# Performance work log

Hardware: AMD Instinct MI355X
Metric: run time of the kernel (lower is better)

Reference implementation:

```python
import jax, jax.numpy as jnp
import numpy as np

META_DIM, CIN, COUT, K = 32, 64, 64, 3
B, N, S = 32, 256, 64


def setup_inputs() -> dict:
    key = jax.random.key(0)
    k1, k2, k3, k4, k5, k6 = jax.random.split(key, 6)
    scale = 1.0 / np.sqrt(META_DIM)
    return {
        "meta_knowledge": jax.random.normal(k1, (B, N, META_DIM), dtype=jnp.float32),
        "x": jax.random.normal(k2, (B, N, S, CIN), dtype=jnp.float32),
        "w_lin_w": jax.random.normal(k3, (CIN * COUT * K, META_DIM), dtype=jnp.float32) * scale,
        "w_lin_b": jax.random.normal(k4, (CIN * COUT * K,), dtype=jnp.float32) * scale,
        "b_lin_w": jax.random.normal(k5, (COUT, META_DIM), dtype=jnp.float32) * scale,
        "b_lin_b": jax.random.normal(k6, (COUT,), dtype=jnp.float32) * scale,
    }


def reference(meta_knowledge, x, w_lin_w, w_lin_b, b_lin_w, b_lin_b):
    # meta_knowledge: [B, N, M]; x: [B, N, S, Cin]
    b, n, s, cin = x.shape
    cout = b_lin_w.shape[0]
    k = w_lin_w.shape[0] // (cin * cout)
    s_out = s - k + 1

    # Hypernetwork: per-(batch,node) conv weights and biases
    # w: [B, N, Cout, Cin, K]
    w = (jnp.einsum("bnm,pm->bnp", meta_knowledge, w_lin_w) + w_lin_b)
    w = w.reshape(b, n, cout, cin, k)
    # bias: [B, N, Cout]
    bias = jnp.einsum("bnm,om->bno", meta_knowledge, b_lin_w) + b_lin_b

    # Sliding windows over seq axis (valid conv): [B, N, S_out, K, Cin]
    x_win = jnp.stack([x[:, :, j : j + s_out, :] for j in range(k)], axis=3)

    # Per-group dynamic conv as batched contraction: [B, N, S_out, Cout]
    out = jnp.einsum("bntkc,bnock->bnto", x_win, w) + bias[:, :, None, :]
    return out
```

## Files before the change

kernel.cpp:

```cpp
#include <hip/hip_runtime.h>
#include <hip/hip_bf16.h>


#define BN_TOT   8192
#define C_IN     64
#define C_OUT    64
#define M_DIM    32
#define S_OUT    62

#define NT       8
#define NTHREADS 1024
#define OSTR     104
#define NODESTR  3336
#define WLDSN    (NT * NODESTR)
#define XLDSN    (NT * 64 * 64)
#define DYNB     ((XLDSN + WLDSN) * 2)
#define WLW_ROWS 12288
#define WS_NEED  (WLW_ROWS * M_DIM * 2 + WLW_ROWS * 4)

typedef __attribute__((ext_vector_type(8))) short bf16x8;
typedef __attribute__((ext_vector_type(4))) float f32x4;

static __device__ __forceinline__ short f2bf(float f) {
    return __bfloat16_as_short(__float2bfloat16(f));
}

static __device__ __forceinline__ bf16x8 cvt8(float4 a, float4 b) {
    bf16x8 r;
    r[0] = f2bf(a.x); r[1] = f2bf(a.y); r[2] = f2bf(a.z); r[3] = f2bf(a.w);
    r[4] = f2bf(b.x); r[5] = f2bf(b.y); r[6] = f2bf(b.z); r[7] = f2bf(b.w);
    return r;
}

extern "C" __global__ void wlw_to_bf16(const float* __restrict__ src,
                                       short* __restrict__ dst) {
    const int i = (blockIdx.x * 256 + threadIdx.x) * 8;
    const float4 a = *reinterpret_cast<const float4*>(src + i);
    const float4 b = *reinterpret_cast<const float4*>(src + i + 4);
    *reinterpret_cast<bf16x8*>(dst + i) = cvt8(a, b);
}

extern "C" __global__ void wlb_rearr(const float* __restrict__ wlb,
                                     float* __restrict__ wlbR) {
    const int i = blockIdx.x * 256 + threadIdx.x;
    const int o = i / 192;
    const int r = i - o * 192;
    const int k = r >> 6;
    const int c = r & 63;
    wlbR[i] = wlb[o * 192 + c * 3 + k];
}

template <int USE_WS>
__global__ void __launch_bounds__(NTHREADS, 4)
metaconv_fused(const float* __restrict__ meta,
               const float* __restrict__ x,
               const float* __restrict__ wlw,
               const short* __restrict__ wlwbf,
               const float* __restrict__ wlb,
               const float* __restrict__ wlbR,
               const float* __restrict__ blw,
               const float* __restrict__ blb,
               float* __restrict__ out)
{
    extern __shared__ __align__(16) short dynsm[];
    short* xsh = dynsm;
    short* wsh = dynsm + XLDSN;
    __shared__ float bias_s[NT][C_OUT];

    const int tid   = threadIdx.x;
    const int wave  = tid >> 6;
    const int lane  = tid & 63;
    const int l16   = lane & 15;
    const int g     = lane >> 4;
    const int node  = wave & (NT - 1);
    const int thalf = wave >> 3;
    const int bn0   = blockIdx.x * NT;

    {
        const float* xsrc = x + (size_t)(bn0 + node) * (64 * C_IN);
        short* xdst = xsh + node * 4096;
        const int ts0 = thalf * 32;
        #pragma unroll
        for (int i = 0; i < 4; ++i) {
            const int gi = i * 64 + lane;
            const int tl = ts0 + (gi >> 3);
            const int gr = gi & 7;
            const float4 a = *reinterpret_cast<const float4*>(xsrc + tl * 64 + gr * 8);
            const float4 b = *reinterpret_cast<const float4*>(xsrc + tl * 64 + gr * 8 + 4);
            const int so = (gr * 8) ^ ((tl & 7) << 3);
            *reinterpret_cast<bf16x8*>(xdst + tl * 64 + so) = cvt8(a, b);
        }
    }

    if (tid < NT * C_OUT) {
        const int bnode = tid >> 6;
        const int o     = tid & 63;
        const float* mrow = meta + (size_t)(bn0 + bnode) * M_DIM;
        const float* brow = blw + o * M_DIM;
        float s = blb[o];
        #pragma unroll
        for (int m = 0; m < M_DIM; ++m) s += mrow[m] * brow[m];
        bias_s[bnode][o] = s;
    }

    bf16x8 metaF;
    {
        const float* mp = meta + (size_t)(bn0 + (l16 & (NT - 1))) * M_DIM + g * 8;
        metaF = cvt8(*reinterpret_cast<const float4*>(mp),
                     *reinterpret_cast<const float4*>(mp + 4));
    }

    const f32x4 ZV = {0.f, 0.f, 0.f, 0.f};
    f32x4 acc[2][4];
    #pragma unroll
    for (int t = 0; t < 2; ++t)
        #pragma unroll
        for (int o = 0; o < 4; ++o) acc[t][o] = ZV;

    __syncthreads();

    #pragma unroll 1
    for (int cchunk = 0; cchunk < 2; ++cchunk) {
        const int c0 = cchunk * 32;
        #pragma unroll
        for (int oh = 0; oh < 2; ++oh) {

            #pragma unroll 1
            for (int ou = 0; ou < 2; ++ou) {
                const int o_l = wave * 2 + ou;
                const int og  = oh * 32 + o_l;
                #pragma unroll
                for (int ch = 0; ch < 2; ++ch) {
                    #pragma unroll
                    for (int k = 0; k < 3; ++k) {
                        const int pr = og * 192 + (c0 + ch * 16 + l16) * 3 + k;
                        bf16x8 aF;
                        f32x4 Cf;
                        if constexpr (USE_WS) {
                            aF = *reinterpret_cast<const bf16x8*>(wlwbf + (size_t)pr * M_DIM + g * 8);
                            const float4 cf = *reinterpret_cast<const float4*>(
                                wlbR + (og * 3 + k) * 64 + c0 + ch * 16 + g * 4);
                            Cf[0] = cf.x; Cf[1] = cf.y; Cf[2] = cf.z; Cf[3] = cf.w;
                        } else {
                            const float* wp = wlw + (size_t)pr * M_DIM + g * 8;
                            aF = cvt8(*reinterpret_cast<const float4*>(wp),
                                      *reinterpret_cast<const float4*>(wp + 4));
                            const int cb = c0 + ch * 16 + g * 4;
                            const int pb = og * 192 + k;
                            Cf[0] = wlb[pb + (cb + 0) * 3];
                            Cf[1] = wlb[pb + (cb + 1) * 3];
                            Cf[2] = wlb[pb + (cb + 2) * 3];
                            Cf[3] = wlb[pb + (cb + 3) * 3];
                        }
                        const f32x4 d = __builtin_amdgcn_mfma_f32_16x16x32_bf16(aF, metaF, Cf, 0, 0, 0);
                        if (l16 < NT) {
                            const int off = l16 * NODESTR + o_l * OSTR + k * 32 + ch * 16 + g * 4;
                            *reinterpret_cast<short4*>(&wsh[off]) =
                                make_short4(f2bf(d[0]), f2bf(d[1]), f2bf(d[2]), f2bf(d[3]));
                        }
                    }
                }
            }
            __syncthreads();

            const short* wn = wsh + node * NODESTR;
            const short* xn = xsh + node * 4096;
            bf16x8 B[2][3];
            #pragma unroll
            for (int ol = 0; ol < 2; ++ol)
                #pragma unroll
                for (int k = 0; k < 3; ++k)
                    B[ol][k] = *reinterpret_cast<const bf16x8*>(
                        wn + (ol * 16 + l16) * OSTR + k * 32 + g * 8);

            #pragma unroll
            for (int ttl = 0; ttl < 2; ++ttl) {
                #pragma unroll
                for (int k = 0; k < 3; ++k) {
                    int row = thalf * 32 + ttl * 16 + l16 + k;
                    row = row < 63 ? row : 63;
                    const int so = (c0 + g * 8) ^ ((row & 7) << 3);
                    const bf16x8 A = *reinterpret_cast<const bf16x8*>(
                        xn + row * 64 + so);
                    #pragma unroll
                    for (int ol = 0; ol < 2; ++ol)
                        acc[ttl][oh * 2 + ol] = __builtin_amdgcn_mfma_f32_16x16x32_bf16(
                            A, B[ol][k], acc[ttl][oh * 2 + ol], 0, 0, 0);
                }
            }
            __syncthreads();
        }
    }

    float* ob = out + (size_t)(bn0 + node) * (S_OUT * C_OUT);
    #pragma unroll
    for (int ttl = 0; ttl < 2; ++ttl) {
        #pragma unroll
        for (int ot = 0; ot < 4; ++ot) {
            const int o  = ot * 16 + l16;
            const float bv = bias_s[node][o];
            #pragma unroll
            for (int r = 0; r < 4; ++r) {
                const int t = thalf * 32 + ttl * 16 + g * 4 + r;
                if (t < S_OUT) ob[t * C_OUT + o] = acc[ttl][ot][r] + bv;
            }
        }
    }
}

extern "C" void kernel_launch(void* const* d_in, const int* in_sizes, int n_in,
                              void* d_out, int out_size, void* d_ws, size_t ws_size,
                              hipStream_t stream) {
    const float* meta = (const float*)d_in[0];
    const float* x    = (const float*)d_in[1];
    const float* wlw  = (const float*)d_in[2];
    const float* wlb  = (const float*)d_in[3];
    const float* blw  = (const float*)d_in[4];
    const float* blb  = (const float*)d_in[5];
    float* out = (float*)d_out;
    (void)in_sizes; (void)n_in; (void)out_size;

    short* wlwbf = (short*)d_ws;
    float* wlbR  = (float*)((char*)d_ws + (size_t)WLW_ROWS * M_DIM * 2);

    if (ws_size >= (size_t)WS_NEED) {
        (void)hipFuncSetAttribute((const void*)&metaconv_fused<1>,
                                  hipFuncAttributeMaxDynamicSharedMemorySize, DYNB);
        wlw_to_bf16<<<dim3(WLW_ROWS * M_DIM / (256 * 8)), dim3(256), 0, stream>>>(wlw, wlwbf);
        wlb_rearr<<<dim3(WLW_ROWS / 256), dim3(256), 0, stream>>>(wlb, wlbR);
        metaconv_fused<1><<<dim3(BN_TOT / NT), dim3(NTHREADS), DYNB, stream>>>(
            meta, x, wlw, wlwbf, wlb, wlbR, blw, blb, out);
    } else {
        (void)hipFuncSetAttribute((const void*)&metaconv_fused<0>,
                                  hipFuncAttributeMaxDynamicSharedMemorySize, DYNB);
        metaconv_fused<0><<<dim3(BN_TOT / NT), dim3(NTHREADS), DYNB, stream>>>(
            meta, x, wlw, wlwbf, wlb, wlbR, blw, blb, out);
    }
}
```

Before: 143.0 us.

## Make blocks persistent over four node groups with prefetched x loads

Each block now loops over four consecutive groups of eight nodes, shrinking the grid by a factor of four. The x tile for the next group is loaded into registers during the final compute phase and written to LDS after the current outputs are stored. Barriers are replaced by an LDS-only waitcnt plus s_barrier so global prefetches stay in flight across barriers. This aims to hide global load latency and reduce per-block setup, at the cost of extra registers and less scheduling flexibility across CUs.

```diff
diff --git a/kernel.cpp b/kernel.cpp
--- a/kernel.cpp
+++ b/kernel.cpp
@@ -9,6 +9,7 @@
 #define S_OUT    62
 
 #define NT       8
+#define GRPS     4
 #define NTHREADS 1024
 #define OSTR     104
 #define NODESTR  3336
@@ -30,6 +31,12 @@
     r[0] = f2bf(a.x); r[1] = f2bf(a.y); r[2] = f2bf(a.z); r[3] = f2bf(a.w);
     r[4] = f2bf(b.x); r[5] = f2bf(b.y); r[6] = f2bf(b.z); r[7] = f2bf(b.w);
     return r;
+}
+
+static __device__ __forceinline__ void barrier_lgkm() {
+    asm volatile("s_waitcnt lgkmcnt(0)" ::: "memory");
+    __builtin_amdgcn_s_barrier();
+    asm volatile("" ::: "memory");
 }
 
 extern "C" __global__ void wlw_to_bf16(const float* __restrict__ src,
@@ -74,136 +81,169 @@
     const int g     = lane >> 4;
     const int node  = wave & (NT - 1);
     const int thalf = wave >> 3;
-    const int bn0   = blockIdx.x * NT;
-
-    {
-        const float* xsrc = x + (size_t)(bn0 + node) * (64 * C_IN);
-        short* xdst = xsh + node * 4096;
-        const int ts0 = thalf * 32;
+    const int ts0   = thalf * 32;
+
+    int bn0 = blockIdx.x * (NT * GRPS);
+
+    float4 xr[8];
+    auto stage_load = [&](int bnb) {
+        const float* xsrc = x + (size_t)(bnb + node) * (64 * C_IN);
         #pragma unroll
         for (int i = 0; i < 4; ++i) {
             const int gi = i * 64 + lane;
             const int tl = ts0 + (gi >> 3);
             const int gr = gi & 7;
-            const float4 a = *reinterpret_cast<const float4*>(xsrc + tl * 64 + gr * 8);
-            const float4 b = *reinterpret_cast<const float4*>(xsrc + tl * 64 + gr * 8 + 4);
+            xr[2 * i]     = *reinterpret_cast<const float4*>(xsrc + tl * 64 + gr * 8);
+            xr[2 * i + 1] = *reinterpret_cast<const float4*>(xsrc + tl * 64 + gr * 8 + 4);
+        }
+    };
+    auto stage_write = [&]() {
+        short* xdst = xsh + node * 4096;
+        #pragma unroll
+        for (int i = 0; i < 4; ++i) {
+            const int gi = i * 64 + lane;
+            const int tl = ts0 + (gi >> 3);
+            const int gr = gi & 7;
             const int so = (gr * 8) ^ ((tl & 7) << 3);
-            *reinterpret_cast<bf16x8*>(xdst + tl * 64 + so) = cvt8(a, b);
-        }
-    }
-
-    if (tid < NT * C_OUT) {
-        const int bnode = tid >> 6;
-        const int o     = tid & 63;
-        const float* mrow = meta + (size_t)(bn0 + bnode) * M_DIM;
-        const float* brow = blw + o * M_DIM;
-        float s = blb[o];
-        #pragma unroll
-        for (int m = 0; m < M_DIM; ++m) s += mrow[m] * brow[m];
-        bias_s[bnode][o] = s;
-    }
+            *reinterpret_cast<bf16x8*>(xdst + tl * 64 + so) = cvt8(xr[2 * i], xr[2 * i + 1]);
+        }
+    };
+
+    auto calc_bias = [&](int bnb) {
+        if (tid < NT * C_OUT) {
+            const int bnode = tid >> 6;
+            const int o     = tid & 63;
+            const float* mrow = meta + (size_t)(bnb + bnode) * M_DIM;
+            const float* brow = blw + o * M_DIM;
+            float s = blb[o];
+            #pragma unroll
+            for (int m = 0; m < M_DIM; ++m) s += mrow[m] * brow[m];
+            bias_s[bnode][o] = s;
+        }
+    };
+    auto load_metaF = [&](int bnb) -> bf16x8 {
+        const float* mp = meta + (size_t)(bnb + (l16 & (NT - 1))) * M_DIM + g * 8;
+        return cvt8(*reinterpret_cast<const float4*>(mp),
+                    *reinterpret_cast<const float4*>(mp + 4));
+    };
 
     bf16x8 metaF;
-    {
-        const float* mp = meta + (size_t)(bn0 + (l16 & (NT - 1))) * M_DIM + g * 8;
-        metaF = cvt8(*reinterpret_cast<const float4*>(mp),
-                     *reinterpret_cast<const float4*>(mp + 4));
-    }
+
+    stage_load(bn0);
+    calc_bias(bn0);
+    metaF = load_metaF(bn0);
+    stage_write();
+    barrier_lgkm();
 
     const f32x4 ZV = {0.f, 0.f, 0.f, 0.f};
-    f32x4 acc[2][4];
-    #pragma unroll
-    for (int t = 0; t < 2; ++t)
-        #pragma unroll
-        for (int o = 0; o < 4; ++o) acc[t][o] = ZV;
-
-    __syncthreads();
 
     #pragma unroll 1
-    for (int cchunk = 0; cchunk < 2; ++cchunk) {
-        const int c0 = cchunk * 32;
-        #pragma unroll
-        for (int oh = 0; oh < 2; ++oh) {
-
-            #pragma unroll 1
-            for (int ou = 0; ou < 2; ++ou) {
-                const int o_l = wave * 2 + ou;
-                const int og  = oh * 32 + o_l;
-                #pragma unroll
-                for (int ch = 0; ch < 2; ++ch) {
+    for (int grp = 0; grp < GRPS; ++grp) {
+        f32x4 acc[2][4];
+        #pragma unroll
+        for (int t = 0; t < 2; ++t)
+            #pragma unroll
+            for (int o = 0; o < 4; ++o) acc[t][o] = ZV;
+
+        #pragma unroll 1
+        for (int cchunk = 0; cchunk < 2; ++cchunk) {
+            const int c0 = cchunk * 32;
+            #pragma unroll
+            for (int oh = 0; oh < 2; ++oh) {
+
+                #pragma unroll 1
+                for (int ou = 0; ou < 2; ++ou) {
+                    const int o_l = wave * 2 + ou;
+                    const int og  = oh * 32 + o_l;
                     #pragma unroll
-                    for (int k = 0; k < 3; ++k) {
-                        const int pr = og * 192 + (c0 + ch * 16 + l16) * 3 + k;
-                        bf16x8 aF;
-                        f32x4 Cf;
-                        if constexpr (USE_WS) {
-                            aF = *reinterpret_cast<const bf16x8*>(wlwbf + (size_t)pr * M_DIM + g * 8);
-                            const float4 cf = *reinterpret_cast<const float4*>(
-                                wlbR + (og * 3 + k) * 64 + c0 + ch * 16 + g * 4);
-                            Cf[0] = cf.x; Cf[1] = cf.y; Cf[2] = cf.z; Cf[3] = cf.w;
-                        } else {
-                            const float* wp = wlw + (size_t)pr * M_DIM + g * 8;
-                            aF = cvt8(*reinterpret_cast<const float4*>(wp),
-                                      *reinterpret_cast<const float4*>(wp + 4));
-                            const int cb = c0 + ch * 16 + g * 4;
-                            const int pb = og * 192 + k;
-                            Cf[0] = wlb[pb + (cb + 0) * 3];
-                            Cf[1] = wlb[pb + (cb + 1) * 3];
-                            Cf[2] = wlb[pb + (cb + 2) * 3];
-                            Cf[3] = wlb[pb + (cb + 3) * 3];
-                        }
-                        const f32x4 d = __builtin_amdgcn_mfma_f32_16x16x32_bf16(aF, metaF, Cf, 0, 0, 0);
-                        if (l16 < NT) {
-                            const int off = l16 * NODESTR + o_l * OSTR + k * 32 + ch * 16 + g * 4;
-                            *reinterpret_cast<short4*>(&wsh[off]) =
-                                make_short4(f2bf(d[0]), f2bf(d[1]), f2bf(d[2]), f2bf(d[3]));
+                    for (int ch = 0; ch < 2; ++ch) {
+                        #pragma unroll
+                        for (int k = 0; k < 3; ++k) {
+                            const int pr = og * 192 + (c0 + ch * 16 + l16) * 3 + k;
+                            bf16x8 aF;
+                            f32x4 Cf;
+                            if constexpr (USE_WS) {
+                                aF = *reinterpret_cast<const bf16x8*>(wlwbf + (size_t)pr * M_DIM + g * 8);
+                                const float4 cf = *reinterpret_cast<const float4*>(
+                                    wlbR + (og * 3 + k) * 64 + c0 + ch * 16 + g * 4);
+                                Cf[0] = cf.x; Cf[1] = cf.y; Cf[2] = cf.z; Cf[3] = cf.w;
+                            } else {
+                                const float* wp = wlw + (size_t)pr * M_DIM + g * 8;
+                                aF = cvt8(*reinterpret_cast<const float4*>(wp),
+                                          *reinterpret_cast<const float4*>(wp + 4));
+                                const int cb = c0 + ch * 16 + g * 4;
+                                const int pb = og * 192 + k;
+                                Cf[0] = wlb[pb + (cb + 0) * 3];
+                                Cf[1] = wlb[pb + (cb + 1) * 3];
+                                Cf[2] = wlb[pb + (cb + 2) * 3];
+                                Cf[3] = wlb[pb + (cb + 3) * 3];
+                            }
+                            const f32x4 d = __builtin_amdgcn_mfma_f32_16x16x32_bf16(aF, metaF, Cf, 0, 0, 0);
+                            if (l16 < NT) {
+                                const int off = l16 * NODESTR + o_l * OSTR + k * 32 + ch * 16 + g * 4;
+                                *reinterpret_cast<short4*>(&wsh[off]) =
+                                    make_short4(f2bf(d[0]), f2bf(d[1]), f2bf(d[2]), f2bf(d[3]));
+                            }
                         }
                     }
                 }
+
+                if (cchunk == 1 && oh == 1 && grp != GRPS - 1)
+                    stage_load(bn0 + NT);
+
+                barrier_lgkm();
+
+                const short* wn = wsh + node * NODESTR;
+                const short* xn = xsh + node * 4096;
+                bf16x8 B[2][3];
+                #pragma unroll
+                for (int ol = 0; ol < 2; ++ol)
+                    #pragma unroll
+                    for (int k = 0; k < 3; ++k)
+                        B[ol][k] = *reinterpret_cast<const bf16x8*>(
+                            wn + (ol * 16 + l16) * OSTR + k * 32 + g * 8);
+
+                #pragma unroll
+                for (int ttl = 0; ttl < 2; ++ttl) {
+                    #pragma unroll
+                    for (int k = 0; k < 3; ++k) {
+                        int row = thalf * 32 + ttl * 16 + l16 + k;
+                        row = row < 63 ? row : 63;
+                        const int so = (c0 + g * 8) ^ ((row & 7) << 3);
+                        const bf16x8 A = *reinterpret_cast<const bf16x8*>(
+                            xn + row * 64 + so);
+                        #pragma unroll
+                        for (int ol = 0; ol < 2; ++ol)
+                            acc[ttl][oh * 2 + ol] = __builtin_amdgcn_mfma_f32_16x16x32_bf16(
+                                A, B[ol][k], acc[ttl][oh * 2 + ol], 0, 0, 0);
+                    }
+                }
+                barrier_lgkm();
             }
-            __syncthreads();
-
-            const short* wn = wsh + node * NODESTR;
-            const short* xn = xsh + node * 4096;
-            bf16x8 B[2][3];
-            #pragma unroll
-            for (int ol = 0; ol < 2; ++ol)
+        }
+
+        float* ob = out + (size_t)(bn0 + node) * (S_OUT * C_OUT);
+        #pragma unroll
+        for (int ttl = 0; ttl < 2; ++ttl) {
+            #pragma unroll
+            for (int ot = 0; ot < 4; ++ot) {
+                const int o  = ot * 16 + l16;
+                const float bv = bias_s[node][o];
                 #pragma unroll
-                for (int k = 0; k < 3; ++k)
-                    B[ol][k] = *reinterpret_cast<const bf16x8*>(
-                        wn + (ol * 16 + l16) * OSTR + k * 32 + g * 8);
-
-            #pragma unroll
-            for (int ttl = 0; ttl < 2; ++ttl) {
-                #pragma unroll
-                for (int k = 0; k < 3; ++k) {
-                    int row = thalf * 32 + ttl * 16 + l16 + k;
-                    row = row < 63 ? row : 63;
-                    const int so = (c0 + g * 8) ^ ((row & 7) << 3);
-                    const bf16x8 A = *reinterpret_cast<const bf16x8*>(
-                        xn + row * 64 + so);
-                    #pragma unroll
-                    for (int ol = 0; ol < 2; ++ol)
-                        acc[ttl][oh * 2 + ol] = __builtin_amdgcn_mfma_f32_16x16x32_bf16(
-                            A, B[ol][k], acc[ttl][oh * 2 + ol], 0, 0, 0);
+                for (int r = 0; r < 4; ++r) {
+                    const int t = thalf * 32 + ttl * 16 + g * 4 + r;
+                    if (t < S_OUT) ob[t * C_OUT + o] = acc[ttl][ot][r] + bv;
                 }
             }
-            __syncthreads();
-        }
-    }
-
-    float* ob = out + (size_t)(bn0 + node) * (S_OUT * C_OUT);
-    #pragma unroll
-    for (int ttl = 0; ttl < 2; ++ttl) {
-        #pragma unroll
-        for (int ot = 0; ot < 4; ++ot) {
-            const int o  = ot * 16 + l16;
-            const float bv = bias_s[node][o];
-            #pragma unroll
-            for (int r = 0; r < 4; ++r) {
-                const int t = thalf * 32 + ttl * 16 + g * 4 + r;
-                if (t < S_OUT) ob[t * C_OUT + o] = acc[ttl][ot][r] + bv;
-            }
+        }
+
+        if (grp != GRPS - 1) {
+            barrier_lgkm();
+            bn0 += NT;
+            calc_bias(bn0);
+            metaF = load_metaF(bn0);
+            stage_write();
+            barrier_lgkm();
         }
     }
 }
@@ -223,17 +263,19 @@
     short* wlwbf = (short*)d_ws;
     float* wlbR  = (float*)((char*)d_ws + (size_t)WLW_ROWS * M_DIM * 2);
 
+    const int grid = BN_TOT / (NT * GRPS);
+
     if (ws_size >= (size_t)WS_NEED) {
         (void)hipFuncSetAttribute((const void*)&metaconv_fused<1>,
                                   hipFuncAttributeMaxDynamicSharedMemorySize, DYNB);
         wlw_to_bf16<<<dim3(WLW_ROWS * M_DIM / (256 * 8)), dim3(256), 0, stream>>>(wlw, wlwbf);
         wlb_rearr<<<dim3(WLW_ROWS / 256), dim3(256), 0, stream>>>(wlb, wlbR);
-        metaconv_fused<1><<<dim3(BN_TOT / NT), dim3(NTHREADS), DYNB, stream>>>(
+        metaconv_fused<1><<<dim3(grid), dim3(NTHREADS), DYNB, stream>>>(
             meta, x, wlw, wlwbf, wlb, wlbR, blw, blb, out);
     } else {
         (void)hipFuncSetAttribute((const void*)&metaconv_fused<0>,
                                   hipFuncAttributeMaxDynamicSharedMemorySize, DYNB);
-        metaconv_fused<0><<<dim3(BN_TOT / NT), dim3(NTHREADS), DYNB, stream>>>(
+        metaconv_fused<0><<<dim3(grid), dim3(NTHREADS), DYNB, stream>>>(
             meta, x, wlw, wlwbf, wlb, wlbR, blw, blb, out);
     }
 }
```

Measured after the change: 199.6 us. 1.4x slower.
